# Performance work log

Measured on AMD Instinct MI355X. Metric: run time of the kernel, lower is better.

The kernel has to match this reference:

```python
import jax, jax.numpy as jnp
import numpy as np

N_NODES = 100000
N_EDGES = 3200000


def _gcn_layer(x, W, b, src, dst, n_nodes):
    # GCNConv: x' = D^{-1/2} (A + I) D^{-1/2} X W + b  (self-loops included in src/dst)
    h = x @ W  # [N, F_out]
    ones = jnp.ones(src.shape[0], dtype=x.dtype)
    deg = jax.ops.segment_sum(ones, dst, num_segments=n_nodes)  # in-degree incl. self-loop
    dinv = jnp.where(deg > 0, jax.lax.rsqrt(deg), 0.0)
    norm = dinv[src] * dinv[dst]  # [E+N]
    msg = h[src] * norm[:, None]  # gather + scale
    out = jax.ops.segment_sum(msg, dst, num_segments=n_nodes)  # scatter-add
    return out + b


def setup_inputs() -> dict:
    key = jax.random.key(0)
    k1, k2, k3, k4 = jax.random.split(key, 4)
    x = jax.random.normal(k1, (N_NODES, 64), dtype=jnp.float32)
    edge_index = jax.random.randint(k2, (2, N_EDGES), 0, N_NODES, dtype=jnp.int64)
    W1 = jax.random.normal(k3, (64, 128), dtype=jnp.float32) * (1.0 / np.sqrt(64))
    b1 = jnp.zeros((128,), dtype=jnp.float32)
    W2 = jax.random.normal(k4, (128, 64), dtype=jnp.float32) * (1.0 / np.sqrt(128))
    b2 = jnp.zeros((64,), dtype=jnp.float32)
    return {"x": x, "edge_index": edge_index, "W1": W1, "b1": b1, "W2": W2, "b2": b2}


def reference(x, edge_index, W1, b1, W2, b2):
    n = x.shape[0]
    loop = jnp.arange(n, dtype=edge_index.dtype)
    src = jnp.concatenate([edge_index[0], loop])
    dst = jnp.concatenate([edge_index[1], loop])
    h = _gcn_layer(x, W1, b1, src, dst, n)
    h = jax.nn.relu(h)
    # dropout is identity in eval mode (training=False)
    out = _gcn_layer(h, W2, b2, src, dst, n)
    return out
```

## Files before the change

### kernel.cpp

```cpp
#include <hip/hip_runtime.h>
#include <hip/hip_fp16.h>

#define N_NODES 100000
#define N_EDGES 3200000

#define NBLK_P 320
#define SLICE4 (N_EDGES / 4 / NBLK_P)
#define NBKT 256
#define BSHIFT 9
#define NBKT_USED ((N_NODES + 511) / 512)

struct alignas(8) Half4 { __half2 lo, hi; };


__global__ __launch_bounds__(256) void k_coarse_hist(const int4* __restrict__ dst4,
                                                     int* __restrict__ blockHist) {
    __shared__ int h[NBKT];
    int t = threadIdx.x;
    h[t] = 0;
    __syncthreads();
    int base = blockIdx.x * SLICE4;
    for (int i = t; i < SLICE4; i += 256) {
        int4 d = dst4[base + i];
        atomicAdd(&h[d.x >> BSHIFT], 1);
        atomicAdd(&h[d.y >> BSHIFT], 1);
        atomicAdd(&h[d.z >> BSHIFT], 1);
        atomicAdd(&h[d.w >> BSHIFT], 1);
    }
    __syncthreads();
    blockHist[blockIdx.x * NBKT + t] = h[t];
}

__global__ __launch_bounds__(256) void k_colscan(int* __restrict__ blockHist,
                                                 int* __restrict__ coarseStart) {
    __shared__ int s[NBKT];
    int t = threadIdx.x;
    int tot = 0;
    for (int b = 0; b < NBLK_P; ++b) tot += blockHist[b * NBKT + t];
    s[t] = tot;
    __syncthreads();
    for (int off = 1; off < NBKT; off <<= 1) {
        int v = (t >= off) ? s[t - off] : 0;
        __syncthreads();
        s[t] += v;
        __syncthreads();
    }
    int cs = s[t] - tot;
    coarseStart[t] = cs;
    if (t == NBKT - 1) coarseStart[NBKT] = s[t];
    int run = cs;
    for (int b = 0; b < NBLK_P; ++b) {
        int v = blockHist[b * NBKT + t];
        blockHist[b * NBKT + t] = run;
        run += v;
    }
}

__global__ __launch_bounds__(256) void k_partition(const int4* __restrict__ src4,
                                                   const int4* __restrict__ dst4,
                                                   const int* __restrict__ blockHist,
                                                   int2* __restrict__ sorted) {
    __shared__ int cur[NBKT];
    int t = threadIdx.x;
    cur[t] = blockHist[blockIdx.x * NBKT + t];
    __syncthreads();
    int base = blockIdx.x * SLICE4;
    for (int i = t; i < SLICE4; i += 256) {
        int4 d = dst4[base + i];
        int4 s = src4[base + i];
        int p;
        p = atomicAdd(&cur[d.x >> BSHIFT], 1); sorted[p] = make_int2(s.x, d.x);
        p = atomicAdd(&cur[d.y >> BSHIFT], 1); sorted[p] = make_int2(s.y, d.y);
        p = atomicAdd(&cur[d.z >> BSHIFT], 1); sorted[p] = make_int2(s.z, d.z);
        p = atomicAdd(&cur[d.w >> BSHIFT], 1); sorted[p] = make_int2(s.w, d.w);
    }
}

__global__ __launch_bounds__(256) void k_fine(const int2* __restrict__ sorted,
                                              const int* __restrict__ coarseStart,
                                              int* __restrict__ rowstart,
                                              float* __restrict__ dinv,
                                              int* __restrict__ csr_src) {
    __shared__ int h[512];
    __shared__ int pairsc[256];
    __shared__ int offs[512];
    int t = threadIdx.x;
    int bkt = blockIdx.x;
    int beg = coarseStart[bkt], end = coarseStart[bkt + 1];
    h[t] = 0; h[t + 256] = 0;
    __syncthreads();
    for (int i = beg + t; i < end; i += 256) {
        int d = sorted[i].y;
        atomicAdd(&h[d & 511], 1);
    }
    __syncthreads();
    int pv = h[2 * t] + h[2 * t + 1];
    pairsc[t] = pv;
    __syncthreads();
    for (int off = 1; off < 256; off <<= 1) {
        int v = (t >= off) ? pairsc[t - off] : 0;
        __syncthreads();
        pairsc[t] += v;
        __syncthreads();
    }
    int e0 = pairsc[t] - pv;
    offs[2 * t] = e0;
    offs[2 * t + 1] = e0 + h[2 * t];
    __syncthreads();
    int n0 = bkt << BSHIFT;
#pragma unroll
    for (int q = 0; q < 2; ++q) {
        int local = t + q * 256;
        int node = n0 + local;
        if (node < N_NODES) {
            rowstart[node] = beg + offs[local];
            dinv[node] = rsqrtf((float)(h[local] + 1));
        }
    }
    if (bkt == 0 && t == 0) rowstart[N_NODES] = N_EDGES;
    __syncthreads();
    for (int i = beg + t; i < end; i += 256) {
        int2 e = sorted[i];
        int p = atomicAdd(&offs[e.y & 511], 1);
        csr_src[beg + p] = e.x;
    }
}


__global__ void k_scale_h4(const float4* __restrict__ in, const float* __restrict__ dinv,
                           Half4* __restrict__ out) {
    long long t = (long long)blockIdx.x * blockDim.x + threadIdx.x;
    if (t >= (long long)N_NODES * 16) return;
    float d = dinv[(int)(t >> 4)];
    float4 v = in[t];
    Half4 h;
    h.lo = __float22half2_rn(make_float2(v.x * d, v.y * d));
    h.hi = __float22half2_rn(make_float2(v.z * d, v.w * d));
    out[t] = h;
}


__global__ __launch_bounds__(256) void k_gather_h(
    const int* __restrict__ rowstart, const int* __restrict__ csr_src,
    const float* __restrict__ dinv, const Half4* __restrict__ xs4,
    const float4* __restrict__ bias4, float4* __restrict__ out4)
{
    int node = blockIdx.x * 4 + (threadIdx.x >> 6);
    if (node >= N_NODES) return;
    int lane = threadIdx.x & 63;
    int qlane = lane & 15;
    int egrp = lane >> 4;
    int beg = rowstart[node];
    int deg = rowstart[node + 1] - beg;
    float4 acc = make_float4(0.f, 0.f, 0.f, 0.f);
    if (egrp == 0) {
        Half4 v = xs4[(long long)node * 16 + qlane];
        float2 a = __half22float2(v.lo), b = __half22float2(v.hi);
        acc.x = a.x; acc.y = a.y; acc.z = b.x; acc.w = b.y;
    }
    for (int base = 0; base < deg; base += 64) {
        int rem = deg - base;
        if (rem > 64) rem = 64;
        int mye = (lane < rem) ? csr_src[beg + base + lane] : 0;
        int nj = (rem + 3) >> 2;
        for (int j = 0; j < nj; ++j) {
            int eidx = (j << 2) + egrp;
            int s = __shfl(mye, eidx);
            if (eidx < rem) {
                Half4 v = xs4[(long long)s * 16 + qlane];
                float2 a = __half22float2(v.lo), b = __half22float2(v.hi);
                acc.x += a.x; acc.y += a.y; acc.z += b.x; acc.w += b.y;
            }
        }
    }
    acc.x += __shfl_xor(acc.x, 16); acc.y += __shfl_xor(acc.y, 16);
    acc.z += __shfl_xor(acc.z, 16); acc.w += __shfl_xor(acc.w, 16);
    acc.x += __shfl_xor(acc.x, 32); acc.y += __shfl_xor(acc.y, 32);
    acc.z += __shfl_xor(acc.z, 32); acc.w += __shfl_xor(acc.w, 32);
    if (egrp == 0) {
        float d = dinv[node];
        float4 b = bias4 ? bias4[qlane] : make_float4(0.f, 0.f, 0.f, 0.f);
        float4 o;
        o.x = d * acc.x + b.x;
        o.y = d * acc.y + b.y;
        o.z = d * acc.z + b.z;
        o.w = d * acc.w + b.w;
        out4[(long long)node * 16 + qlane] = o;
    }
}


#define GTILE 128
__global__ __launch_bounds__(256) void k_fused_gemm(
    const float* __restrict__ A, const float* __restrict__ W1,
    const float* __restrict__ b1, const float* __restrict__ W2,
    const float* __restrict__ dinv, Half4* __restrict__ P)
{
    __shared__ float sBuf[128][GTILE];
    int tid = threadIdx.x;
    int R0 = blockIdx.x * GTILE;

    {
        int row = tid >> 1;
        int kb = (tid & 1) * 32;
        int grow = R0 + row;
        if (grow < N_NODES) {
            const float4* src = (const float4*)&A[(long long)grow * 64 + kb];
#pragma unroll
            for (int q = 0; q < 8; ++q) {
                float4 v = src[q];
                int k = kb + q * 4;
                sBuf[k + 0][row] = v.x;
                sBuf[k + 1][row] = v.y;
                sBuf[k + 2][row] = v.z;
                sBuf[k + 3][row] = v.w;
            }
        } else {
#pragma unroll
            for (int q = 0; q < 8; ++q) {
                int k = kb + q * 4;
                sBuf[k + 0][row] = 0.f; sBuf[k + 1][row] = 0.f;
                sBuf[k + 2][row] = 0.f; sBuf[k + 3][row] = 0.f;
            }
        }
    }
    __syncthreads();

    int rg = tid & 15;
    int cg = tid >> 4;
    int r0 = rg * 8;

    float acc[8][8];
#pragma unroll
    for (int i = 0; i < 8; ++i)
#pragma unroll
        for (int j = 0; j < 8; ++j) acc[i][j] = 0.f;
    {
        int c0 = cg * 8;
#pragma unroll 4
        for (int k = 0; k < 64; ++k) {
            float4 a0 = *(const float4*)&sBuf[k][r0];
            float4 a1 = *(const float4*)&sBuf[k][r0 + 4];
            float4 w0 = *(const float4*)&W1[k * 128 + c0];
            float4 w1 = *(const float4*)&W1[k * 128 + c0 + 4];
            float av[8] = {a0.x, a0.y, a0.z, a0.w, a1.x, a1.y, a1.z, a1.w};
            float wv[8] = {w0.x, w0.y, w0.z, w0.w, w1.x, w1.y, w1.z, w1.w};
#pragma unroll
            for (int i = 0; i < 8; ++i)
#pragma unroll
                for (int j = 0; j < 8; ++j) acc[i][j] += av[i] * wv[j];
        }
    }
    __syncthreads();

    {
        int c0 = cg * 8;
#pragma unroll
        for (int j = 0; j < 8; ++j) {
            float bb = b1[c0 + j];
            float4 h0, h1;
            h0.x = fmaxf(acc[0][j] + bb, 0.f);
            h0.y = fmaxf(acc[1][j] + bb, 0.f);
            h0.z = fmaxf(acc[2][j] + bb, 0.f);
            h0.w = fmaxf(acc[3][j] + bb, 0.f);
            h1.x = fmaxf(acc[4][j] + bb, 0.f);
            h1.y = fmaxf(acc[5][j] + bb, 0.f);
            h1.z = fmaxf(acc[6][j] + bb, 0.f);
            h1.w = fmaxf(acc[7][j] + bb, 0.f);
            *(float4*)&sBuf[c0 + j][r0] = h0;
            *(float4*)&sBuf[c0 + j][r0 + 4] = h1;
        }
    }
    __syncthreads();

    {
        int c0 = cg * 4;
        float acc2[8][4];
#pragma unroll
        for (int i = 0; i < 8; ++i)
#pragma unroll
            for (int j = 0; j < 4; ++j) acc2[i][j] = 0.f;
#pragma unroll 4
        for (int k = 0; k < 128; ++k) {
            float4 a0 = *(const float4*)&sBuf[k][r0];
            float4 a1 = *(const float4*)&sBuf[k][r0 + 4];
            float4 w = *(const float4*)&W2[k * 64 + c0];
            float av[8] = {a0.x, a0.y, a0.z, a0.w, a1.x, a1.y, a1.z, a1.w};
            float wv[4] = {w.x, w.y, w.z, w.w};
#pragma unroll
            for (int i = 0; i < 8; ++i)
#pragma unroll
                for (int j = 0; j < 4; ++j) acc2[i][j] += av[i] * wv[j];
        }
#pragma unroll
        for (int i = 0; i < 8; ++i) {
            int row = R0 + r0 + i;
            if (row < N_NODES) {
                float d = dinv[row];
                Half4 h;
                h.lo = __float22half2_rn(make_float2(d * acc2[i][0], d * acc2[i][1]));
                h.hi = __float22half2_rn(make_float2(d * acc2[i][2], d * acc2[i][3]));
                P[(long long)row * 16 + cg] = h;
            }
        }
    }
}


extern "C" void kernel_launch(void* const* d_in, const int* in_sizes, int n_in,
                              void* d_out, int out_size, void* d_ws, size_t ws_size,
                              hipStream_t stream) {
    const float* x  = (const float*)d_in[0];
    const int*   ei = (const int*)d_in[1];
    const float* W1 = (const float*)d_in[2];
    const float* b1 = (const float*)d_in[3];
    const float* W2 = (const float*)d_in[4];
    const float* b2 = (const float*)d_in[5];
    float* out = (float*)d_out;

    const int* srcE = ei;
    const int* dstE = ei + N_EDGES;

    char* w = (char*)d_ws;
    int*   blockHist   = (int*)w;   w += sizeof(int) * NBLK_P * NBKT;
    int*   coarseStart = (int*)w;   w += sizeof(int) * (NBKT + 1);
    int*   rowstart    = (int*)w;   w += sizeof(int) * (N_NODES + 8);
    float* dinv        = (float*)w; w += sizeof(float) * (N_NODES + 8);
    int*   csr_src     = (int*)w;   w += sizeof(int) * N_EDGES;
    Half4* xs          = (Half4*)w; w += sizeof(Half4) * (size_t)N_NODES * 16;
    int2*  sorted      = (int2*)w;
    float* agg1        = (float*)w; w += sizeof(float) * (size_t)N_NODES * 64;
    Half4* p2 = xs;

    const int B = 256;
    int gNF4 = (int)(((long long)N_NODES * 16 + B - 1) / B);

    k_coarse_hist<<<NBLK_P, 256, 0, stream>>>((const int4*)dstE, blockHist);
    k_colscan<<<1, 256, 0, stream>>>(blockHist, coarseStart);
    k_partition<<<NBLK_P, 256, 0, stream>>>((const int4*)srcE, (const int4*)dstE,
                                            blockHist, sorted);
    k_fine<<<NBKT_USED, 256, 0, stream>>>(sorted, coarseStart, rowstart, dinv, csr_src);

    k_scale_h4<<<gNF4, B, 0, stream>>>((const float4*)x, dinv, xs);
    k_gather_h<<<(N_NODES + 3) / 4, 256, 0, stream>>>(rowstart, csr_src, dinv,
                                                      xs, nullptr, (float4*)agg1);
    k_fused_gemm<<<(N_NODES + GTILE - 1) / GTILE, 256, 0, stream>>>(agg1, W1, b1, W2, dinv, p2);

    k_gather_h<<<(N_NODES + 3) / 4, 256, 0, stream>>>(rowstart, csr_src, dinv,
                                                      p2, (const float4*)b2, (float4*)out);
}
```

Before: 344.4 us.

## Pack sorted edges, stage buckets in LDS, fuse scaling, widen gather loads

Edges are packed into one int (17-bit src plus 9-bit local dst), which halves the partition writes and fine-pass reads. The fine pass keeps each bucket in LDS when it fits, so global memory is read once instead of twice. The separate x-scale kernel is folded into the fine kernel, which saves a launch and a dinv reread. The column scan uses 1024 threads to spread the serial per-block loops, and the gather loads 16-byte int4 rows so 8 edges are in flight per wave instead of 4. Risks are lower occupancy from the large LDS buffer in the fine kernel, and packing that assumes node ids below 2^17.

New measurement: 314.0 us. 8.8% less time.

```diff
diff --git a/kernel.cpp b/kernel.cpp
--- a/kernel.cpp
+++ b/kernel.cpp
@@ -9,6 +9,7 @@
 #define NBKT 256
 #define BSHIFT 9
 #define NBKT_USED ((N_NODES + 511) / 512)
+#define EL_CAP 24576
 
 struct alignas(8) Half4 { __half2 lo, hi; };
 
@@ -31,27 +32,43 @@
     blockHist[blockIdx.x * NBKT + t] = h[t];
 }
 
-__global__ __launch_bounds__(256) void k_colscan(int* __restrict__ blockHist,
-                                                 int* __restrict__ coarseStart) {
+__global__ __launch_bounds__(1024) void k_colscan(int* __restrict__ blockHist,
+                                                  int* __restrict__ coarseStart) {
+    __shared__ int part[4][NBKT];
     __shared__ int s[NBKT];
-    int t = threadIdx.x;
-    int tot = 0;
-    for (int b = 0; b < NBLK_P; ++b) tot += blockHist[b * NBKT + t];
-    s[t] = tot;
+    __shared__ int totA[NBKT];
+    int tid = threadIdx.x;
+    int b = tid & 255, q = tid >> 8;
+    const int QR = NBLK_P / 4;
+    int sum = 0;
+    for (int r = q * QR; r < (q + 1) * QR; ++r) sum += blockHist[r * NBKT + b];
+    part[q][b] = sum;
+    __syncthreads();
+    if (q == 0) {
+        int tot = part[0][b] + part[1][b] + part[2][b] + part[3][b];
+        s[b] = tot;
+        totA[b] = tot;
+    }
     __syncthreads();
     for (int off = 1; off < NBKT; off <<= 1) {
-        int v = (t >= off) ? s[t - off] : 0;
-        __syncthreads();
-        s[t] += v;
-        __syncthreads();
-    }
-    int cs = s[t] - tot;
-    coarseStart[t] = cs;
-    if (t == NBKT - 1) coarseStart[NBKT] = s[t];
-    int run = cs;
-    for (int b = 0; b < NBLK_P; ++b) {
-        int v = blockHist[b * NBKT + t];
-        blockHist[b * NBKT + t] = run;
+        int v = 0;
+        if (q == 0 && b >= off) v = s[b - off];
+        __syncthreads();
+        if (q == 0) s[b] += v;
+        __syncthreads();
+    }
+    int excl = s[b] - totA[b];
+    if (q == 0) {
+        coarseStart[b] = excl;
+        if (b == 0) coarseStart[NBKT] = N_EDGES;
+    }
+    int run = excl;
+    if (q > 0) run += part[0][b];
+    if (q > 1) run += part[1][b];
+    if (q > 2) run += part[2][b];
+    for (int r = q * QR; r < (q + 1) * QR; ++r) {
+        int v = blockHist[r * NBKT + b];
+        blockHist[r * NBKT + b] = run;
         run += v;
     }
 }
@@ -59,7 +76,7 @@
 __global__ __launch_bounds__(256) void k_partition(const int4* __restrict__ src4,
                                                    const int4* __restrict__ dst4,
                                                    const int* __restrict__ blockHist,
-                                                   int2* __restrict__ sorted) {
+                                                   int* __restrict__ sorted) {
     __shared__ int cur[NBKT];
     int t = threadIdx.x;
     cur[t] = blockHist[blockIdx.x * NBKT + t];
@@ -69,29 +86,38 @@
         int4 d = dst4[base + i];
         int4 s = src4[base + i];
         int p;
-        p = atomicAdd(&cur[d.x >> BSHIFT], 1); sorted[p] = make_int2(s.x, d.x);
-        p = atomicAdd(&cur[d.y >> BSHIFT], 1); sorted[p] = make_int2(s.y, d.y);
-        p = atomicAdd(&cur[d.z >> BSHIFT], 1); sorted[p] = make_int2(s.z, d.z);
-        p = atomicAdd(&cur[d.w >> BSHIFT], 1); sorted[p] = make_int2(s.w, d.w);
-    }
-}
-
-__global__ __launch_bounds__(256) void k_fine(const int2* __restrict__ sorted,
+        p = atomicAdd(&cur[d.x >> BSHIFT], 1); sorted[p] = s.x | ((d.x & 511) << 17);
+        p = atomicAdd(&cur[d.y >> BSHIFT], 1); sorted[p] = s.y | ((d.y & 511) << 17);
+        p = atomicAdd(&cur[d.z >> BSHIFT], 1); sorted[p] = s.z | ((d.z & 511) << 17);
+        p = atomicAdd(&cur[d.w >> BSHIFT], 1); sorted[p] = s.w | ((d.w & 511) << 17);
+    }
+}
+
+__global__ __launch_bounds__(256) void k_fine(const int* __restrict__ sorted,
                                               const int* __restrict__ coarseStart,
+                                              const float4* __restrict__ x4,
                                               int* __restrict__ rowstart,
-                                              float* __restrict__ dinv,
-                                              int* __restrict__ csr_src) {
+                                              float* __restrict__ dinvg,
+                                              int* __restrict__ csr_src,
+                                              Half4* __restrict__ xs) {
+    __shared__ int eL[EL_CAP];
     __shared__ int h[512];
     __shared__ int pairsc[256];
     __shared__ int offs[512];
+    __shared__ float dloc[512];
     int t = threadIdx.x;
     int bkt = blockIdx.x;
     int beg = coarseStart[bkt], end = coarseStart[bkt + 1];
+    int cnt = end - beg;
+    bool inLds = (cnt <= EL_CAP);
     h[t] = 0; h[t + 256] = 0;
     __syncthreads();
-    for (int i = beg + t; i < end; i += 256) {
-        int d = sorted[i].y;
-        atomicAdd(&h[d & 511], 1);
+    if (inLds) {
+        for (int i = t; i < cnt; i += 256) eL[i] = sorted[beg + i];
+        __syncthreads();
+        for (int i = t; i < cnt; i += 256) atomicAdd(&h[eL[i] >> 17], 1);
+    } else {
+        for (int i = beg + t; i < end; i += 256) atomicAdd(&h[sorted[i] >> 17], 1);
     }
     __syncthreads();
     int pv = h[2 * t] + h[2 * t + 1];
@@ -108,84 +134,103 @@
     offs[2 * t + 1] = e0 + h[2 * t];
     __syncthreads();
     int n0 = bkt << BSHIFT;
+    int nvalid = N_NODES - n0;
+    if (nvalid > 512) nvalid = 512;
 #pragma unroll
     for (int q = 0; q < 2; ++q) {
         int local = t + q * 256;
-        int node = n0 + local;
-        if (node < N_NODES) {
-            rowstart[node] = beg + offs[local];
-            dinv[node] = rsqrtf((float)(h[local] + 1));
+        if (local < nvalid) {
+            rowstart[n0 + local] = beg + offs[local];
+            float dv = rsqrtf((float)(h[local] + 1));
+            dloc[local] = dv;
+            dinvg[n0 + local] = dv;
         }
     }
     if (bkt == 0 && t == 0) rowstart[N_NODES] = N_EDGES;
     __syncthreads();
-    for (int i = beg + t; i < end; i += 256) {
-        int2 e = sorted[i];
-        int p = atomicAdd(&offs[e.y & 511], 1);
-        csr_src[beg + p] = e.x;
-    }
-}
-
-
-__global__ void k_scale_h4(const float4* __restrict__ in, const float* __restrict__ dinv,
-                           Half4* __restrict__ out) {
-    long long t = (long long)blockIdx.x * blockDim.x + threadIdx.x;
-    if (t >= (long long)N_NODES * 16) return;
-    float d = dinv[(int)(t >> 4)];
-    float4 v = in[t];
-    Half4 h;
-    h.lo = __float22half2_rn(make_float2(v.x * d, v.y * d));
-    h.hi = __float22half2_rn(make_float2(v.z * d, v.w * d));
-    out[t] = h;
+    if (inLds) {
+        for (int i = t; i < cnt; i += 256) {
+            int pk = eL[i];
+            int p = atomicAdd(&offs[pk >> 17], 1);
+            csr_src[beg + p] = pk & 0x1FFFF;
+        }
+    } else {
+        for (int i = beg + t; i < end; i += 256) {
+            int pk = sorted[i];
+            int p = atomicAdd(&offs[pk >> 17], 1);
+            csr_src[beg + p] = pk & 0x1FFFF;
+        }
+    }
+    for (int i = t; i < nvalid * 16; i += 256) {
+        int local = i >> 4;
+        int qq = i & 15;
+        float d = dloc[local];
+        float4 v = x4[(long long)(n0 + local) * 16 + qq];
+        Half4 hh;
+        hh.lo = __float22half2_rn(make_float2(v.x * d, v.y * d));
+        hh.hi = __float22half2_rn(make_float2(v.z * d, v.w * d));
+        xs[(long long)(n0 + local) * 16 + qq] = hh;
+    }
 }
 
 
 __global__ __launch_bounds__(256) void k_gather_h(
     const int* __restrict__ rowstart, const int* __restrict__ csr_src,
-    const float* __restrict__ dinv, const Half4* __restrict__ xs4,
+    const float* __restrict__ dinv, const int4* __restrict__ xs16,
     const float4* __restrict__ bias4, float4* __restrict__ out4)
 {
     int node = blockIdx.x * 4 + (threadIdx.x >> 6);
     if (node >= N_NODES) return;
     int lane = threadIdx.x & 63;
-    int qlane = lane & 15;
-    int egrp = lane >> 4;
+    int qlane = lane & 7;
+    int egrp = lane >> 3;
     int beg = rowstart[node];
     int deg = rowstart[node + 1] - beg;
-    float4 acc = make_float4(0.f, 0.f, 0.f, 0.f);
+    float acc[8];
+#pragma unroll
+    for (int k = 0; k < 8; ++k) acc[k] = 0.f;
     if (egrp == 0) {
-        Half4 v = xs4[(long long)node * 16 + qlane];
-        float2 a = __half22float2(v.lo), b = __half22float2(v.hi);
-        acc.x = a.x; acc.y = a.y; acc.z = b.x; acc.w = b.y;
+        int4 v = xs16[((long long)node << 3) + qlane];
+        float2 f0 = __half22float2(*(__half2*)&v.x);
+        float2 f1 = __half22float2(*(__half2*)&v.y);
+        float2 f2 = __half22float2(*(__half2*)&v.z);
+        float2 f3 = __half22float2(*(__half2*)&v.w);
+        acc[0] = f0.x; acc[1] = f0.y; acc[2] = f1.x; acc[3] = f1.y;
+        acc[4] = f2.x; acc[5] = f2.y; acc[6] = f3.x; acc[7] = f3.y;
     }
     for (int base = 0; base < deg; base += 64) {
         int rem = deg - base;
         if (rem > 64) rem = 64;
         int mye = (lane < rem) ? csr_src[beg + base + lane] : 0;
-        int nj = (rem + 3) >> 2;
+        int nj = (rem + 7) >> 3;
         for (int j = 0; j < nj; ++j) {
-            int eidx = (j << 2) + egrp;
+            int eidx = (j << 3) + egrp;
             int s = __shfl(mye, eidx);
             if (eidx < rem) {
-                Half4 v = xs4[(long long)s * 16 + qlane];
-                float2 a = __half22float2(v.lo), b = __half22float2(v.hi);
-                acc.x += a.x; acc.y += a.y; acc.z += b.x; acc.w += b.y;
+                int4 v = xs16[((long long)s << 3) + qlane];
+                float2 f0 = __half22float2(*(__half2*)&v.x);
+                float2 f1 = __half22float2(*(__half2*)&v.y);
+                float2 f2 = __half22float2(*(__half2*)&v.z);
+                float2 f3 = __half22float2(*(__half2*)&v.w);
+                acc[0] += f0.x; acc[1] += f0.y; acc[2] += f1.x; acc[3] += f1.y;
+                acc[4] += f2.x; acc[5] += f2.y; acc[6] += f3.x; acc[7] += f3.y;
             }
         }
     }
-    acc.x += __shfl_xor(acc.x, 16); acc.y += __shfl_xor(acc.y, 16);
-    acc.z += __shfl_xor(acc.z, 16); acc.w += __shfl_xor(acc.w, 16);
-    acc.x += __shfl_xor(acc.x, 32); acc.y += __shfl_xor(acc.y, 32);
-    acc.z += __shfl_xor(acc.z, 32); acc.w += __shfl_xor(acc.w, 32);
+#pragma unroll
+    for (int k = 0; k < 8; ++k) {
+        acc[k] += __shfl_xor(acc[k], 8);
+        acc[k] += __shfl_xor(acc[k], 16);
+        acc[k] += __shfl_xor(acc[k], 32);
+    }
     if (egrp == 0) {
         float d = dinv[node];
-        float4 b = bias4 ? bias4[qlane] : make_float4(0.f, 0.f, 0.f, 0.f);
-        float4 o;
-        o.x = d * acc.x + b.x;
-        o.y = d * acc.y + b.y;
-        o.z = d * acc.z + b.z;
-        o.w = d * acc.w + b.w;
-        out4[(long long)node * 16 + qlane] = o;
+        float4 b0 = bias4 ? bias4[qlane * 2] : make_float4(0.f, 0.f, 0.f, 0.f);
+        float4 b1 = bias4 ? bias4[qlane * 2 + 1] : make_float4(0.f, 0.f, 0.f, 0.f);
+        out4[(long long)node * 16 + qlane * 2] =
+            make_float4(d * acc[0] + b0.x, d * acc[1] + b0.y, d * acc[2] + b0.z, d * acc[3] + b0.w);
+        out4[(long long)node * 16 + qlane * 2 + 1] =
+            make_float4(d * acc[4] + b1.x, d * acc[5] + b1.y, d * acc[6] + b1.z, d * acc[7] + b1.w);
     }
 }
 
@@ -328,24 +373,23 @@
     float* dinv        = (float*)w; w += sizeof(float) * (N_NODES + 8);
     int*   csr_src     = (int*)w;   w += sizeof(int) * N_EDGES;
     Half4* xs          = (Half4*)w; w += sizeof(Half4) * (size_t)N_NODES * 16;
-    int2*  sorted      = (int2*)w;
+    int*   sorted      = (int*)w;
     float* agg1        = (float*)w; w += sizeof(float) * (size_t)N_NODES * 64;
     Half4* p2 = xs;
 
-    const int B = 256;
-    int gNF4 = (int)(((long long)N_NODES * 16 + B - 1) / B);
-
     k_coarse_hist<<<NBLK_P, 256, 0, stream>>>((const int4*)dstE, blockHist);
-    k_colscan<<<1, 256, 0, stream>>>(blockHist, coarseStart);
+    k_colscan<<<1, 1024, 0, stream>>>(blockHist, coarseStart);
     k_partition<<<NBLK_P, 256, 0, stream>>>((const int4*)srcE, (const int4*)dstE,
                                             blockHist, sorted);
-    k_fine<<<NBKT_USED, 256, 0, stream>>>(sorted, coarseStart, rowstart, dinv, csr_src);
-
-    k_scale_h4<<<gNF4, B, 0, stream>>>((const float4*)x, dinv, xs);
+    k_fine<<<NBKT_USED, 256, 0, stream>>>(sorted, coarseStart, (const float4*)x,
+                                          rowstart, dinv, csr_src, xs);
+
     k_gather_h<<<(N_NODES + 3) / 4, 256, 0, stream>>>(rowstart, csr_src, dinv,
-                                                      xs, nullptr, (float4*)agg1);
+                                                      (const int4*)xs, nullptr,
+                                                      (float4*)agg1);
     k_fused_gemm<<<(N_NODES + GTILE - 1) / GTILE, 256, 0, stream>>>(agg1, W1, b1, W2, dinv, p2);
 
     k_gather_h<<<(N_NODES + 3) / 4, 256, 0, stream>>>(rowstart, csr_src, dinv,
-                                                      p2, (const float4*)b2, (float4*)out);
-}
+                                                      (const int4*)p2, (const float4*)b2,
+                                                      (float4*)out);
+}
```
